# Performance work log

Measured on AMD Instinct MI355X. Metric: run time of the kernel, lower is better.

The kernel has to match this reference:

```python
import jax, jax.numpy as jnp
import numpy as np

B, T, C, H = 8, 1024, 768, 12
HD = C // H  # head_dim = 64


def setup_inputs() -> dict:
    key = jax.random.key(0)
    ks = jax.random.split(key, 5)
    x = jax.random.normal(ks[0], (B, T, C), dtype=jnp.float32)
    mask = jnp.tril(jnp.ones((T, T), dtype=bool))[None, None, :, :]  # causal [1,1,T,T]
    # Dense params (flax Dense: y = x @ kernel + bias)
    W_qkv = jax.random.normal(ks[1], (C, 3 * C), dtype=jnp.float32) * (1.0 / np.sqrt(C))
    b_qkv = jnp.zeros((3 * C,), dtype=jnp.float32)
    W_proj = jax.random.normal(ks[2], (C, C), dtype=jnp.float32) * (1.0 / np.sqrt(C))
    b_proj = jnp.zeros((C,), dtype=jnp.float32)
    return {"x": x, "mask": mask, "W_qkv": W_qkv, "b_qkv": b_qkv,
            "W_proj": W_proj, "b_proj": b_proj}


def reference(x, mask, W_qkv, b_qkv, W_proj, b_proj):
    Bx, Tx, Cx = x.shape
    qkv = x @ W_qkv + b_qkv                      # [B, T, 3C]
    qkv = qkv.reshape(Bx, Tx, 3 * H, HD)
    q, k, v = jnp.array_split(qkv, 3, axis=2)    # each [B, T, H, HD]
    scale = 1.0 / jnp.sqrt(jnp.float32(HD))
    attn = jnp.einsum('bqhd,bkhd->bhqk', q, k) * scale  # [B, H, T, T]
    attn = jnp.where(mask, attn, jnp.finfo(jnp.float32).min)
    attn = jax.nn.softmax(attn, axis=-1)
    out = jnp.einsum('bhqk,bkhd->bqhd', attn, v).reshape(Bx, Tx, Cx)
    return out @ W_proj + b_proj
```

## Files before the change

kernel.cpp:

```cpp
#include <hip/hip_runtime.h>


typedef unsigned short u16;
typedef unsigned int u32;
typedef __bf16 bf16x8 __attribute__((ext_vector_type(8)));
typedef float  f32x4  __attribute__((ext_vector_type(4)));
typedef float  f32x16 __attribute__((ext_vector_type(16)));
typedef unsigned short u16x4 __attribute__((ext_vector_type(4)));
typedef unsigned short u16x8 __attribute__((ext_vector_type(8)));

#define DEV static __device__ __forceinline__

constexpr int B_ = 8, T_ = 1024, C_ = 768, H_ = 12, HD_ = 64;
constexpr int M1 = B_ * T_;
constexpr int N1 = 3 * C_;
constexpr int KD = C_;

DEV u16 f2bf(float f) {
    union { float f; unsigned u; } v; v.f = f;
    unsigned r = v.u + 0x7fffu + ((v.u >> 16) & 1u);
    return (u16)(r >> 16);
}

DEV u16 bfbits(float f) {
    __bf16 h = (__bf16)f;
    union { __bf16 h; u16 u; } v; v.h = h;
    return v.u;
}

DEV void gload16(const void* g, void* l) {
    __builtin_amdgcn_global_load_lds(
        (const __attribute__((address_space(1))) unsigned*)g,
        (__attribute__((address_space(3))) unsigned*)l, 16, 0, 0);
}

DEV float redmax16(f32x16 v) {
    float a0 = fmaxf(v[0], v[1]), a1 = fmaxf(v[2], v[3]);
    float a2 = fmaxf(v[4], v[5]), a3 = fmaxf(v[6], v[7]);
    float a4 = fmaxf(v[8], v[9]), a5 = fmaxf(v[10], v[11]);
    float a6 = fmaxf(v[12], v[13]), a7 = fmaxf(v[14], v[15]);
    float b0 = fmaxf(a0, a1), b1 = fmaxf(a2, a3);
    float b2 = fmaxf(a4, a5), b3 = fmaxf(a6, a7);
    return fmaxf(fmaxf(b0, b1), fmaxf(b2, b3));
}
DEV float redsum16(f32x16 v) {
    float a0 = v[0] + v[1], a1 = v[2] + v[3], a2 = v[4] + v[5], a3 = v[6] + v[7];
    float a4 = v[8] + v[9], a5 = v[10] + v[11], a6 = v[12] + v[13], a7 = v[14] + v[15];
    float b0 = a0 + a1, b1 = a2 + a3, b2 = a4 + a5, b3 = a6 + a7;
    return (b0 + b1) + (b2 + b3);
}


__global__ __launch_bounds__(256) void cvt_x_kern(const float* __restrict__ x,
                                                  u16* __restrict__ xb, int n8) {
    int i = blockIdx.x * 256 + threadIdx.x;
    if (i >= n8) return;
    const float4* xf = (const float4*)x;
    float4 a = xf[i * 2], b = xf[i * 2 + 1];
    u16x8 o;
    o[0] = f2bf(a.x); o[1] = f2bf(a.y); o[2] = f2bf(a.z); o[3] = f2bf(a.w);
    o[4] = f2bf(b.x); o[5] = f2bf(b.y); o[6] = f2bf(b.z); o[7] = f2bf(b.w);
    *(u16x8*)(xb + (size_t)i * 8) = o;
}

__global__ __launch_bounds__(256) void cvt_w_kern(const float* __restrict__ Wq,
                                                  const float* __restrict__ Wp,
                                                  u16* __restrict__ WqT,
                                                  u16* __restrict__ WpT) {
    __shared__ float tile[32][33];
    int bx = blockIdx.x;
    const float* W; u16* Wt; int N;
    if (bx < N1 / 32) { W = Wq; Wt = WqT; N = N1; }
    else { bx -= N1 / 32; W = Wp; Wt = WpT; N = C_; }
    int n0 = bx * 32, k0 = blockIdx.y * 32;
    int tx = threadIdx.x & 31, ty = threadIdx.x >> 5;
#pragma unroll
    for (int i = 0; i < 4; i++) {
        int k = ty * 4 + i;
        tile[k][tx] = W[(size_t)(k0 + k) * N + n0 + tx];
    }
    __syncthreads();
#pragma unroll
    for (int i = 0; i < 4; i++) {
        int n = ty * 4 + i;
        Wt[(size_t)(n0 + n) * KD + k0 + tx] = f2bf(tile[tx][n]);
    }
}


template <int MODE>
__global__ __launch_bounds__(256, 2) void gemm_bt_kern(
    const u16* __restrict__ A, const u16* __restrict__ Bt,
    const float* __restrict__ bias, int nBN,
    u16* __restrict__ qw, u16* __restrict__ kw, u16* __restrict__ vw,
    float* __restrict__ out) {
    __shared__ u16 lds[16384];
    char* LA = (char*)lds;
    char* LB = (char*)lds + 16384;
    const int cpx = gridDim.x >> 3;
    const int bid = (blockIdx.x & 7) * cpx + (blockIdx.x >> 3);
    const int bm = bid / nBN, bn = bid % nBN;
    const int m0 = bm * 128, n0 = bn * 128;
    const int t = threadIdx.x;
    const int lane = t & 63, w = t >> 6;
    const int wr = w >> 1, wc = w & 1;
    const int l15 = lane & 15, lhi = lane >> 4;
    const int srow = t >> 3;
    const int scb = ((t & 7) << 4) ^ ((srow & 7) << 4);
    const char* Ab = (const char*)(A + (size_t)(m0 + srow) * KD) + scb;
    const char* Bb = (const char*)(Bt + (size_t)(n0 + srow) * KD) + scb;

    f32x4 acc[4][4] = {};

    for (int k0 = 0; k0 < KD; k0 += 64) {
#pragma unroll
        for (int s = 0; s < 4; s++) {
            gload16(Ab + (size_t)k0 * 2 + (size_t)s * 32 * KD * 2, LA + w * 1024 + s * 4096);
            gload16(Bb + (size_t)k0 * 2 + (size_t)s * 32 * KD * 2, LB + w * 1024 + s * 4096);
        }
        __syncthreads();
#pragma unroll
        for (int kk = 0; kk < 2; kk++) {
            bf16x8 af[4], bfr[4];
#pragma unroll
            for (int i = 0; i < 4; i++) {
                int rowA = wr * 64 + i * 16 + l15;
                af[i] = *(const bf16x8*)(LA + rowA * 128 +
                                         ((kk * 64 + lhi * 16) ^ ((rowA & 7) << 4)));
                int rowB = wc * 64 + i * 16 + l15;
                bfr[i] = *(const bf16x8*)(LB + rowB * 128 +
                                          ((kk * 64 + lhi * 16) ^ ((rowB & 7) << 4)));
            }
#pragma unroll
            for (int fm = 0; fm < 4; fm++)
#pragma unroll
                for (int fn = 0; fn < 4; fn++)
                    acc[fm][fn] = __builtin_amdgcn_mfma_f32_16x16x32_bf16(
                        af[fm], bfr[fn], acc[fm][fn], 0, 0, 0);
        }
        __syncthreads();
    }

    if constexpr (MODE == 1) {
#pragma unroll
        for (int fm = 0; fm < 4; fm++) {
            const int mb = m0 + wr * 64 + fm * 16 + lhi * 4;
#pragma unroll
            for (int fn = 0; fn < 4; fn++) {
                const int n = n0 + wc * 64 + fn * 16 + l15;
                const float bv = bias[n];
#pragma unroll
                for (int r = 0; r < 4; r++)
                    out[(size_t)(mb + r) * C_ + n] = acc[fm][fn][r] + bv;
            }
        }
    } else {
        char* TT = (char*)lds;
        const int typ = bn / 6;
        const int h0 = (bn % 6) * 2;
        if (typ < 2) {
            const float sc = (typ == 0) ? 0.125f : 1.0f;
#pragma unroll
            for (int fn = 0; fn < 4; fn++) {
                const int col = wc * 64 + fn * 16 + l15;
                const float bv = bias[n0 + col];
#pragma unroll
                for (int fm = 0; fm < 4; fm++) {
                    const int row0 = wr * 64 + fm * 16 + lhi * 4;
#pragma unroll
                    for (int r = 0; r < 4; r++) {
                        const int row = row0 + r;
                        *(u16*)(TT + row * 256 + ((col * 2) ^ ((row & 7) << 5))) =
                            bfbits((acc[fm][fn][r] + bv) * sc);
                    }
                }
            }
            __syncthreads();
            u16* dst = (typ == 0) ? qw : kw;
#pragma unroll
            for (int i = 0; i < 8; i++) {
                const int wk = t + 256 * i;
                const int m = wk >> 4, c = wk & 15;
                u16x8 v8 = *(u16x8*)(TT + m * 256 + ((c * 16) ^ ((m & 7) << 5)));
                const int mb = m0 + m, b = mb >> 10, tq = mb & 1023;
                const int h = h0 + (c >> 3), d0 = (c & 7) * 8;
                *(u16x8*)(dst + (((size_t)(b * H_ + h) * T_ + tq) << 6) + d0) = v8;
            }
        } else {
#pragma unroll
            for (int fn = 0; fn < 4; fn++) {
                const int col = wc * 64 + fn * 16 + l15;
                const float bv = bias[n0 + col];
                const int cx = (col & 7) << 4;
#pragma unroll
                for (int fm = 0; fm < 4; fm++) {
                    const int row0 = wr * 64 + fm * 16 + lhi * 4;
                    u16x4 pk;
#pragma unroll
                    for (int r = 0; r < 4; r++) pk[r] = bfbits(acc[fm][fn][r] + bv);
                    *(u16x4*)(TT + col * 256 + ((row0 * 2) ^ cx)) = pk;
                }
            }
            __syncthreads();
#pragma unroll
            for (int i = 0; i < 8; i++) {
                const int wk = t + 256 * i;
                const int col = wk >> 4, ch = wk & 15;
                u16x8 v8 = *(u16x8*)(TT + col * 256 + ((ch * 16) ^ ((col & 7) << 4)));
                const int b = m0 >> 10, tq0 = (m0 & 1023) + ch * 8;
                const int h = h0 + (col >> 6), d = col & 63;
                *(u16x8*)(vw + (((size_t)(b * H_ + h) * HD_ + d) << 10) + tq0) = v8;
            }
        }
    }
}


__global__ __launch_bounds__(256, 3) void attn_fwd_kern(
    const u16* __restrict__ qg, const u16* __restrict__ kg,
    const u16* __restrict__ vg, u16* __restrict__ ao) {
    __shared__ u16 kld[2][64 * 64];
    __shared__ u16 vld[2][64 * 64];
    __shared__ u16 pld[4][32 * 64];
    const int n = blockIdx.x;
    const int bh = (n & 7) + 8 * ((n >> 3) % 12);
    const int qt = 7 - n / 96;
    const int t = threadIdx.x, lane = t & 63, w = t >> 6;
    const int q5 = lane & 31, h2 = lane >> 5;
    const int srow = t >> 3;
    const int scb = ((t & 7) << 4) ^ ((srow & 7) << 4);
    const char* kb = (const char*)(kg + (size_t)bh * T_ * HD_);
    const char* vb = (const char*)(vg + (size_t)bh * HD_ * T_);

    const int qrow_g = qt * 128 + w * 32 + q5;
    const u16* qrow = qg + (size_t)bh * T_ * HD_ + (size_t)qrow_g * HD_ + h2 * 8;
    bf16x8 qf[4];
#pragma unroll
    for (int kc = 0; kc < 4; kc++)
        qf[kc] = *(const bf16x8*)(qrow + kc * 16);

#pragma unroll
    for (int s = 0; s < 2; s++) {
        gload16(kb + (size_t)(srow + s * 32) * 128 + scb,
                (char*)kld[0] + w * 1024 + s * 4096);
        gload16(vb + (size_t)(srow + s * 32) * 2048 + scb,
                (char*)vld[0] + w * 1024 + s * 4096);
    }
    __syncthreads();

    f32x16 acc[2] = {};
    float mst = -1e30f, lst = 0.f;
    const int qmax = qt * 128 + w * 32 + 31;
    char* pw = (char*)pld[w];

    const int ntiles = 2 * qt + 2;
    for (int kvt = 0; kvt < ntiles; kvt++) {
        const int cur = kvt & 1;
        if (kvt + 1 < ntiles) {
#pragma unroll
            for (int s = 0; s < 2; s++) {
                gload16(kb + (size_t)((kvt + 1) * 64 + srow + s * 32) * 128 + scb,
                        (char*)kld[cur ^ 1] + w * 1024 + s * 4096);
                gload16(vb + (size_t)(srow + s * 32) * 2048 + (kvt + 1) * 128 + scb,
                        (char*)vld[cur ^ 1] + w * 1024 + s * 4096);
            }
        }
        if (kvt * 64 <= qmax) {
            const char* kbase = (const char*)kld[cur];
            const char* vbase = (const char*)vld[cur];
            f32x16 s0 = {}, s1 = {};
            __builtin_amdgcn_s_setprio(1);
#pragma unroll
            for (int kc = 0; kc < 4; kc++) {
                const int r0 = q5, r1 = 32 + q5;
                bf16x8 kf0 = *(const bf16x8*)(kbase + r0 * 128 +
                                              ((kc * 32 + h2 * 16) ^ ((r0 & 7) << 4)));
                bf16x8 kf1 = *(const bf16x8*)(kbase + r1 * 128 +
                                              ((kc * 32 + h2 * 16) ^ ((r1 & 7) << 4)));
                s0 = __builtin_amdgcn_mfma_f32_32x32x16_bf16(kf0, qf[kc], s0, 0, 0, 0);
                s1 = __builtin_amdgcn_mfma_f32_32x32x16_bf16(kf1, qf[kc], s1, 0, 0, 0);
            }
            __builtin_amdgcn_s_setprio(0);
            if (kvt * 64 + 63 > qt * 128 + w * 32) {
                const int qg_ = qrow_g, kvb0 = kvt * 64 + 4 * h2;
#pragma unroll
                for (int r = 0; r < 16; r++) {
                    const int kvo = (r & 3) + 8 * (r >> 2);
                    if (kvb0 + kvo > qg_) s0[r] = -1e30f;
                    if (kvb0 + 32 + kvo > qg_) s1[r] = -1e30f;
                }
            }
            float pmax = fmaxf(redmax16(s0), redmax16(s1));
            pmax = fmaxf(pmax, __shfl_xor(pmax, 32));
            const float mn = fmaxf(mst, pmax);
            const float corr = __expf(mst - mn);
            mst = mn;
#pragma unroll
            for (int r = 0; r < 16; r++) {
                s0[r] = __expf(s0[r] - mn);
                s1[r] = __expf(s1[r] - mn);
            }
            float rs = redsum16(s0) + redsum16(s1);
            rs += __shfl_xor(rs, 32);
            lst = lst * corr + rs;
#pragma unroll
            for (int r = 0; r < 16; r++) { acc[0][r] *= corr; acc[1][r] *= corr; }
            const int swz = (q5 & 7) << 4;
#pragma unroll
            for (int a = 0; a < 8; a++) {
                const int kv0 = ((2 * a) & 3) + 8 * (a >> 1) + 4 * h2;
                u32 pk0 = (u32)bfbits(s0[2 * a]) | ((u32)bfbits(s0[2 * a + 1]) << 16);
                u32 pk1 = (u32)bfbits(s1[2 * a]) | ((u32)bfbits(s1[2 * a + 1]) << 16);
                *(u32*)(pw + q5 * 128 + ((kv0 * 2) ^ swz)) = pk0;
                *(u32*)(pw + q5 * 128 + (((kv0 + 32) * 2) ^ swz)) = pk1;
            }
            bf16x8 pf[4];
#pragma unroll
            for (int m = 0; m < 4; m++)
                pf[m] = *(const bf16x8*)(pw + q5 * 128 + ((m * 32 + h2 * 16) ^ swz));
            __builtin_amdgcn_s_setprio(1);
#pragma unroll
            for (int m = 0; m < 4; m++) {
#pragma unroll
                for (int db = 0; db < 2; db++) {
                    const int rd = db * 32 + q5;
                    bf16x8 vf = *(const bf16x8*)(vbase + rd * 128 +
                                                 ((m * 32 + h2 * 16) ^ ((rd & 7) << 4)));
                    acc[db] = __builtin_amdgcn_mfma_f32_32x32x16_bf16(vf, pf[m], acc[db], 0, 0, 0);
                }
            }
            __builtin_amdgcn_s_setprio(0);
        }
        __syncthreads();
    }

    const int b = bh / H_, h = bh % H_;
    const float inv = 1.0f / lst;
    u16* orow = ao + (size_t)(b * T_ + qrow_g) * C_ + h * 64 + 4 * h2;
#pragma unroll
    for (int db = 0; db < 2; db++)
#pragma unroll
        for (int q2 = 0; q2 < 4; q2++) {
            u16x4 pk;
#pragma unroll
            for (int e = 0; e < 4; e++) pk[e] = bfbits(acc[db][q2 * 4 + e] * inv);
            *(u16x4*)(orow + db * 32 + q2 * 8) = pk;
        }
}


extern "C" void kernel_launch(void* const* d_in, const int* in_sizes, int n_in,
                              void* d_out, int out_size, void* d_ws, size_t ws_size,
                              hipStream_t stream) {
    const float* x     = (const float*)d_in[0];
    const float* Wqkv  = (const float*)d_in[2];
    const float* bqkv  = (const float*)d_in[3];
    const float* Wproj = (const float*)d_in[4];
    const float* bproj = (const float*)d_in[5];
    float* out = (float*)d_out;

    char* ws = (char*)d_ws;
    u16* xb     = (u16*)(ws);
    u16* wqkvT  = (u16*)(ws + 12582912);
    u16* wprojT = (u16*)(ws + 16121856);
    u16* qw     = (u16*)(ws + 17301504);
    u16* kw     = (u16*)(ws + 29884416);
    u16* vw     = (u16*)(ws + 42467328);
    u16* ao     = (u16*)(ws + 55050240);

    cvt_x_kern<<<(M1 * C_ / 8 + 255) / 256, 256, 0, stream>>>(x, xb, M1 * C_ / 8);
    cvt_w_kern<<<dim3(N1 / 32 + C_ / 32, KD / 32), 256, 0, stream>>>(
        Wqkv, Wproj, wqkvT, wprojT);

    gemm_bt_kern<0><<<(M1 / 128) * (N1 / 128), 256, 0, stream>>>(
        xb, wqkvT, bqkv, N1 / 128, qw, kw, vw, nullptr);

    attn_fwd_kern<<<B_ * H_ * (T_ / 128), 256, 0, stream>>>(qw, kw, vw, ao);

    gemm_bt_kern<1><<<(M1 / 128) * (C_ / 128), 256, 0, stream>>>(
        ao, wprojT, bproj, C_ / 128, nullptr, nullptr, nullptr, out);
}
```

Baseline: 103.6 us.

## Keep P in registers via permlane32 swap, use exp2 and lazy rescaling

```diff
diff --git a/kernel.cpp b/kernel.cpp
--- a/kernel.cpp
+++ b/kernel.cpp
@@ -8,6 +8,7 @@
 typedef float  f32x16 __attribute__((ext_vector_type(16)));
 typedef unsigned short u16x4 __attribute__((ext_vector_type(4)));
 typedef unsigned short u16x8 __attribute__((ext_vector_type(8)));
+typedef unsigned int u32x4 __attribute__((ext_vector_type(4)));
 
 #define DEV static __device__ __forceinline__
 
@@ -26,6 +27,12 @@
     __bf16 h = (__bf16)f;
     union { __bf16 h; u16 u; } v; v.h = h;
     return v.u;
+}
+
+DEV u32 cvtpk(float lo, float hi) {
+    u32 r;
+    asm("v_cvt_pk_bf16_f32 %0, %1, %2" : "=v"(r) : "v"(lo), "v"(hi));
+    return r;
 }
 
 DEV void gload16(const void* g, void* l) {
@@ -159,7 +166,7 @@
         const int typ = bn / 6;
         const int h0 = (bn % 6) * 2;
         if (typ < 2) {
-            const float sc = (typ == 0) ? 0.125f : 1.0f;
+            const float sc = (typ == 0) ? 0.125f * 1.44269504f : 1.0f;
 #pragma unroll
             for (int fn = 0; fn < 4; fn++) {
                 const int col = wc * 64 + fn * 16 + l15;
@@ -216,12 +223,11 @@
 }
 
 
-__global__ __launch_bounds__(256, 3) void attn_fwd_kern(
+__global__ __launch_bounds__(256, 4) void attn_fwd_kern(
     const u16* __restrict__ qg, const u16* __restrict__ kg,
     const u16* __restrict__ vg, u16* __restrict__ ao) {
     __shared__ u16 kld[2][64 * 64];
     __shared__ u16 vld[2][64 * 64];
-    __shared__ u16 pld[4][32 * 64];
     const int n = blockIdx.x;
     const int bh = (n & 7) + 8 * ((n >> 3) % 12);
     const int qt = 7 - n / 96;
@@ -251,7 +257,6 @@
     f32x16 acc[2] = {};
     float mst = -1e30f, lst = 0.f;
     const int qmax = qt * 128 + w * 32 + 31;
-    char* pw = (char*)pld[w];
 
     const int ntiles = 2 * qt + 2;
     for (int kvt = 0; kvt < ntiles; kvt++) {
@@ -292,32 +297,40 @@
             }
             float pmax = fmaxf(redmax16(s0), redmax16(s1));
             pmax = fmaxf(pmax, __shfl_xor(pmax, 32));
-            const float mn = fmaxf(mst, pmax);
-            const float corr = __expf(mst - mn);
-            mst = mn;
+            if (!__all(pmax <= mst)) {
+                const float mn = fmaxf(mst, pmax);
+                const float corr = exp2f(mst - mn);
+                mst = mn;
+#pragma unroll
+                for (int r = 0; r < 16; r++) { acc[0][r] *= corr; acc[1][r] *= corr; }
+                lst *= corr;
+            }
 #pragma unroll
             for (int r = 0; r < 16; r++) {
-                s0[r] = __expf(s0[r] - mn);
-                s1[r] = __expf(s1[r] - mn);
+                s0[r] = exp2f(s0[r] - mst);
+                s1[r] = exp2f(s1[r] - mst);
             }
             float rs = redsum16(s0) + redsum16(s1);
             rs += __shfl_xor(rs, 32);
-            lst = lst * corr + rs;
-#pragma unroll
-            for (int r = 0; r < 16; r++) { acc[0][r] *= corr; acc[1][r] *= corr; }
-            const int swz = (q5 & 7) << 4;
-#pragma unroll
-            for (int a = 0; a < 8; a++) {
-                const int kv0 = ((2 * a) & 3) + 8 * (a >> 1) + 4 * h2;
-                u32 pk0 = (u32)bfbits(s0[2 * a]) | ((u32)bfbits(s0[2 * a + 1]) << 16);
-                u32 pk1 = (u32)bfbits(s1[2 * a]) | ((u32)bfbits(s1[2 * a + 1]) << 16);
-                *(u32*)(pw + q5 * 128 + ((kv0 * 2) ^ swz)) = pk0;
-                *(u32*)(pw + q5 * 128 + (((kv0 + 32) * 2) ^ swz)) = pk1;
+            lst += rs;
+            u32 pw0[8], pw1[8];
+#pragma unroll
+            for (int i = 0; i < 4; i++) {
+                pw0[i]     = cvtpk(s0[4 * i + 0], s0[4 * i + 1]);
+                pw1[i]     = cvtpk(s0[4 * i + 2], s0[4 * i + 3]);
+                pw0[i + 4] = cvtpk(s1[4 * i + 0], s1[4 * i + 1]);
+                pw1[i + 4] = cvtpk(s1[4 * i + 2], s1[4 * i + 3]);
             }
             bf16x8 pf[4];
 #pragma unroll
-            for (int m = 0; m < 4; m++)
-                pf[m] = *(const bf16x8*)(pw + q5 * 128 + ((m * 32 + h2 * 16) ^ swz));
+            for (int m = 0; m < 4; m++) {
+                u32 a0 = pw0[2 * m], b0 = pw0[2 * m + 1];
+                asm("v_permlane32_swap_b32 %0, %1" : "+v"(a0), "+v"(b0));
+                u32 a1 = pw1[2 * m], b1 = pw1[2 * m + 1];
+                asm("v_permlane32_swap_b32 %0, %1" : "+v"(a1), "+v"(b1));
+                u32x4 wv; wv[0] = a0; wv[1] = a1; wv[2] = b0; wv[3] = b1;
+                pf[m] = __builtin_bit_cast(bf16x8, wv);
+            }
             __builtin_amdgcn_s_setprio(1);
 #pragma unroll
             for (int m = 0; m < 4; m++) {
```

Result: no change. 105.0 us (+1.4%).
